# Performance work log

Hardware: AMD Instinct MI355X
Metric: run time of the kernel (lower is better)

## Reference

```python
import jax, jax.numpy as jnp
import numpy as np

H, W = 1280, 1920          # dense depth canvas (hardcoded in the torch module)
OUT_H, OUT_W = 427, 640    # kornia resize target
BIG = 1e9                  # sentinel coordinate for 'no seed yet'
FX = FY = 1000.0
CX, CY = 960.0, 640.0


def _jfa_nearest(valid):
    """1+JFA jump-flooding: (H,W) bool -> (H,W,2) float coords of nearest valid pixel.
    Replaces the faiss GpuIndexFlatL2 exact 1-NN over pixel coordinates."""
    rr, cc = jnp.meshgrid(jnp.arange(H, dtype=jnp.float32),
                          jnp.arange(W, dtype=jnp.float32), indexing='ij')
    coords = jnp.stack([rr, cc], axis=-1)                      # (H,W,2)
    nearest = jnp.where(valid[..., None], coords, BIG)
    best = jnp.sum((coords - nearest) ** 2, axis=-1)           # squared dist to current seed
    row_idx = jnp.arange(H)[:, None]
    col_idx = jnp.arange(W)[None, :]
    steps = [1, 1024, 512, 256, 128, 64, 32, 16, 8, 4, 2, 1]   # 1+JFA schedule, max dim 1920
    for k in steps:
        for dy in (-k, 0, k):
            for dx in (-k, 0, k):
                if dy == 0 and dx == 0:
                    continue
                cand = jnp.roll(nearest, (dy, dx), axis=(0, 1))
                src_r = row_idx - dy
                src_c = col_idx - dx
                ok = (src_r >= 0) & (src_r < H) & (src_c >= 0) & (src_c < W)
                cand = jnp.where(ok[..., None], cand, BIG)
                d = jnp.sum((coords - cand) ** 2, axis=-1)
                better = d < best
                best = jnp.where(better, d, best)
                nearest = jnp.where(better[..., None], cand, nearest)
    return nearest


def _one(points, pose, extrinsic, intrinsic):
    # projection path uses points.detach() in the torch code -> stop_gradient here
    p = jax.lax.stop_gradient(points)
    pts_world = p @ pose[:3, :3].T + pose[:3, 3]
    cam = pts_world @ extrinsic[:3, :3].T + extrinsic[:3, 3]
    proj = cam @ intrinsic.T
    u = proj[:, 0] / proj[:, 2]
    v = proj[:, 1] / proj[:, 2]
    r = jnp.floor(v).astype(jnp.int32)   # indices[..., [1,0]] swap -> row = v
    c = jnp.floor(u).astype(jnp.int32)
    depth_vals = jnp.linalg.norm(points, axis=-1)   # differentiable wrt points
    mask = (r >= 0) & (r < H) & (c >= 0) & (c < W)
    rs = jnp.where(mask, r, 0)
    cs = jnp.where(mask, c, 0)
    vals = jnp.where(mask, depth_vals, 0.0)
    # sparse scatter -> dense (duplicates sum, like torch.sparse to_dense)
    depth = jnp.zeros((H, W), jnp.float32).at[rs, cs].add(vals)
    valid = depth != 0
    nearest = jax.lax.stop_gradient(_jfa_nearest(valid))   # integer NN indices: non-diff
    nr = jnp.clip(nearest[..., 0], 0, H - 1).astype(jnp.int32)
    nc = jnp.clip(nearest[..., 1], 0, W - 1).astype(jnp.int32)
    rrf = jnp.arange(H, dtype=jnp.float32)[:, None]
    ccf = jnp.arange(W, dtype=jnp.float32)[None, :]
    dist = jnp.sqrt((rrf - nr.astype(jnp.float32)) ** 2 + (ccf - nc.astype(jnp.float32)) ** 2)
    dist = jnp.where(valid, 0.0, dist)          # dist_matrix only written at invalid pixels
    filled = jnp.where(valid, depth, depth[nr, nc])  # depth*(1-mask) + interpolated*mask
    out = jnp.stack([filled, dist], axis=0)     # (2, H, W)
    return jax.image.resize(out, (2, OUT_H, OUT_W), method='linear')


_batched = jax.jit(jax.vmap(_one))


def setup_inputs() -> dict:
    key = jax.random.key(0)
    B, N = 2, 120000
    ku, kv, kd = jax.random.split(key, 3)
    # sample pixels + depths, back-project so points land on the canvas
    u = jax.random.uniform(ku, (B, N), minval=0.0, maxval=W - 1.0)
    v = jax.random.uniform(kv, (B, N), minval=0.0, maxval=H - 1.0)
    d = jax.random.uniform(kd, (B, N), minval=2.0, maxval=50.0)
    x = (u - CX) * d / FX
    y = (v - CY) * d / FY
    points = jnp.stack([x, y, d], axis=-1).astype(jnp.float32)
    eye4 = jnp.broadcast_to(jnp.eye(4, dtype=jnp.float32), (B, 4, 4))
    K = jnp.array([[FX, 0.0, CX], [0.0, FY, CY], [0.0, 0.0, 1.0]], jnp.float32)
    intrinsic = jnp.broadcast_to(K, (B, 3, 3))
    return {"points": points, "pose": eye4, "extrinsic": eye4, "intrinsic": intrinsic}


def reference(points, pose, extrinsic, intrinsic):
    return _batched(points, pose, extrinsic, intrinsic)   # (B, 2, 427, 640)
```

## Files before the change

### kernel.cpp

```cpp
#include <hip/hip_runtime.h>
#include <math.h>
#include <limits.h>

#define HH 1280
#define WW 1920
#define OUT_H 427
#define OUT_W 640
#define SENT 0x7fff7fff

typedef short short2v __attribute__((ext_vector_type(2)));

__device__ __forceinline__ int dot22(int a, int P) {
#if __has_builtin(__builtin_amdgcn_sdot2)
    short2v s = __builtin_bit_cast(short2v, a) - __builtin_bit_cast(short2v, P);
    return __builtin_amdgcn_sdot2(s, s, 0, false);
#else
    int dr = (a >> 16) - (P >> 16);
    int dc = (short)a - (short)P;
    return dr * dr + dc * dc;
#endif
}
#define PICK(P, cur, dcur, cand)                    \
    {                                               \
        int _d = dot22((cand), (P));                \
        if (_d < (dcur)) { (cur) = (cand); (dcur) = _d; } \
    }

__global__ void scatter_k(const float* __restrict__ pts,
                          const float* __restrict__ pose,
                          const float* __restrict__ extr,
                          const float* __restrict__ intr,
                          float* __restrict__ depth, int N) {
    #pragma clang fp contract(off)
    int t = blockIdx.x * blockDim.x + threadIdx.x;
    int b = blockIdx.y;
    if (t >= N) return;
    const float* p = pts + ((long)b * N + t) * 3;
    float x = p[0], y = p[1], z = p[2];
    const float* P = pose + b * 16;
    const float* E = extr + b * 16;
    const float* K = intr + b * 9;
    float wx = ((x*P[0] + y*P[1]) + z*P[2]) + P[3];
    float wy = ((x*P[4] + y*P[5]) + z*P[6]) + P[7];
    float wz = ((x*P[8] + y*P[9]) + z*P[10]) + P[11];
    float cx = ((wx*E[0] + wy*E[1]) + wz*E[2]) + E[3];
    float cy = ((wx*E[4] + wy*E[5]) + wz*E[6]) + E[7];
    float cz = ((wx*E[8] + wy*E[9]) + wz*E[10]) + E[11];
    float px = (cx*K[0] + cy*K[1]) + cz*K[2];
    float py = (cx*K[3] + cy*K[4]) + cz*K[5];
    float pz = (cx*K[6] + cy*K[7]) + cz*K[8];
    float u = px / pz, v = py / pz;
    int r = (int)floorf(v), c = (int)floorf(u);
    if (r >= 0 && r < HH && c >= 0 && c < WW) {
        float dv = sqrtf((x*x + y*y) + z*z);
        atomicAdd(depth + ((long)b * HH + r) * WW + c, dv);
    }
}

template <bool FIRST>
__global__ __launch_bounds__(512)
void jfa3r_k(const void* __restrict__ inv_, int* __restrict__ out, int dy, int k) {
    __shared__ int rows[4][WW];
    int i = blockIdx.x, b = blockIdx.y;
    if (FIRST) {
        const float* dep = (const float*)inv_ + (long)b * HH * WW;
        #pragma unroll
        for (int t = 0; t < 4; ++t) {
            int r = i - t * dy;
            if (r >= 0 && r < HH) {
                const float4* src = reinterpret_cast<const float4*>(dep + (long)r * WW);
                for (int c4 = threadIdx.x; c4 < WW / 4; c4 += 512) {
                    float4 d = src[c4];
                    int4 v;
                    int c0 = c4 * 4, pb = r << 16;
                    v.x = (d.x != 0.0f) ? (pb | c0)       : SENT;
                    v.y = (d.y != 0.0f) ? (pb | (c0 + 1)) : SENT;
                    v.z = (d.z != 0.0f) ? (pb | (c0 + 2)) : SENT;
                    v.w = (d.w != 0.0f) ? (pb | (c0 + 3)) : SENT;
                    reinterpret_cast<int4*>(rows[t])[c4] = v;
                }
            } else {
                int4 sv; sv.x = sv.y = sv.z = sv.w = SENT;
                for (int c4 = threadIdx.x; c4 < WW / 4; c4 += 512)
                    reinterpret_cast<int4*>(rows[t])[c4] = sv;
            }
        }
    } else {
        const int* im = (const int*)inv_ + (long)b * HH * WW;
        #pragma unroll
        for (int t = 0; t < 4; ++t) {
            int r = i - t * dy;
            if (r >= 0 && r < HH) {
                const int4* src = reinterpret_cast<const int4*>(im + (long)r * WW);
                for (int c4 = threadIdx.x; c4 < WW / 4; c4 += 512)
                    reinterpret_cast<int4*>(rows[t])[c4] = src[c4];
            } else {
                int4 sv; sv.x = sv.y = sv.z = sv.w = SENT;
                for (int c4 = threadIdx.x; c4 < WW / 4; c4 += 512)
                    reinterpret_cast<int4*>(rows[t])[c4] = sv;
            }
        }
    }
    __syncthreads();
    bool rv1 = (unsigned)(i - dy)     < (unsigned)HH;
    bool rv2 = (unsigned)(i - 2 * dy) < (unsigned)HH;
    int* orow = out + ((long)b * HH + i) * WW;
    for (int j = threadIdx.x; j < WW; j += 512) {
        bool jk = (j + k < WW);
        int Pp = (i << 16) | j;
        int cur = rows[0][j];
        int dcur = dot22(cur, Pp);
        int c1 = jk ? rows[1][j + k] : SENT;
        PICK(Pp, cur, dcur, c1)
        int o1m = SENT;
        if (rv1) {
            int Pm = ((i - dy) << 16) | j;
            int a = rows[1][j];
            int da = dot22(a, Pm);
            int c2 = jk ? rows[2][j + k] : SENT;
            PICK(Pm, a, da, c2)
            o1m = a;
        }
        PICK(Pp, cur, dcur, o1m)
        int o2q = SENT;
        int qj = j - k;
        if (rv1 && qj >= 0) {
            int Pq = ((i - dy) << 16) | qj;
            int a0 = rows[1][qj];
            int d0 = dot22(a0, Pq);
            PICK(Pq, a0, d0, rows[2][j])
            int a1 = SENT;
            if (rv2) {
                int Pq2 = ((i - 2 * dy) << 16) | qj;
                a1 = rows[2][qj];
                int d1 = dot22(a1, Pq2);
                PICK(Pq2, a1, d1, rows[3][j])
            }
            PICK(Pq, a0, d0, a1)
            o2q = a0;
        }
        PICK(Pp, cur, dcur, o2q)
        orow[j] = cur;
    }
}

__global__ __launch_bounds__(512)
void jfa2r_k(const int* __restrict__ in, int* __restrict__ out, int k) {
    __shared__ int row[WW];
    int i = blockIdx.x, b = blockIdx.y;
    const int4* src = reinterpret_cast<const int4*>(in + ((long)b * HH + i) * WW);
    for (int c4 = threadIdx.x; c4 < WW / 4; c4 += 512)
        reinterpret_cast<int4*>(row)[c4] = src[c4];
    __syncthreads();
    int* orow = out + ((long)b * HH + i) * WW;
    for (int j = threadIdx.x; j < WW; j += 512) {
        int Pp = (i << 16) | j;
        int a = row[j];
        int cur = a;
        int dcur = dot22(cur, Pp);
        int apk = (j + k < WW) ? row[j + k] : SENT;
        PICK(Pp, cur, dcur, apk)
        int o1m = SENT;
        int qj = j - k;
        if (qj >= 0) {
            int Pm = (i << 16) | qj;
            int am = row[qj];
            int dm = dot22(am, Pm);
            PICK(Pm, am, dm, a)
            o1m = am;
        }
        PICK(Pp, cur, dcur, o1m)
        orow[j] = cur;
    }
}

__global__ __launch_bounds__(256)
void hresize_k(const float* __restrict__ depth,
               const int* __restrict__ nr,
               float* __restrict__ tmp) {
    __shared__ float fbuf[WW];
    __shared__ float dbuf[WW];
    int i = blockIdx.x, b = blockIdx.y;
    const float* dep = depth + (long)b * HH * WW;
    const float* drow = dep + (long)i * WW;
    const int* nrow = nr + ((long)b * HH + i) * WW;
    for (int j = threadIdx.x; j < WW; j += 256) {
        float dv = drow[j];
        float f, dist;
        if (dv != 0.0f) { f = dv; dist = 0.0f; }
        else {
            int nn = nrow[j];
            int rr, cc;
            if (nn == SENT) { rr = HH - 1; cc = WW - 1; }
            else { rr = nn >> 16; cc = nn & 0xffff; }
            f = dep[(long)rr * WW + cc];
            float drr = (float)i - (float)rr, dcc = (float)j - (float)cc;
            dist = sqrtf(drr * drr + dcc * dcc);
        }
        fbuf[j] = f; dbuf[j] = dist;
    }
    __syncthreads();
    const float inv = 3.0f;
    for (int ow = threadIdx.x; ow < OUT_W; ow += 256) {
        float sf = (ow + 0.5f) * inv - 0.5f;
        int i0 = (int)ceilf(sf - inv);
        float a0 = 0.f, a1 = 0.f, wsum = 0.f;
        for (int k = 0; k < 7; ++k) {
            int iw = i0 + k;
            if (iw < 0 || iw >= WW) continue;
            float wgt = 1.0f - fabsf(sf - (float)iw) / inv;
            if (wgt <= 0.0f) continue;
            a0 += wgt * fbuf[iw]; a1 += wgt * dbuf[iw]; wsum += wgt;
        }
        long o = (((long)b * 2 + 0) * HH + i) * OUT_W + ow;
        tmp[o] = a0 / wsum;
        tmp[o + (long)HH * OUT_W] = a1 / wsum;
    }
}

__global__ void vresize_k(const float* __restrict__ tmp, float* __restrict__ out) {
    int ow = blockIdx.x * blockDim.x + threadIdx.x;
    int oh = blockIdx.y, bc = blockIdx.z;
    if (ow >= OUT_W) return;
    const float inv = (float)(1280.0 / 427.0);
    float sf = (oh + 0.5f) * inv - 0.5f;
    int i0 = (int)ceilf(sf - inv);
    float acc = 0.f, wsum = 0.f;
    const float* src = tmp + (long)bc * HH * OUT_W;
    for (int k = 0; k < 7; ++k) {
        int ih = i0 + k;
        if (ih < 0 || ih >= HH) continue;
        float wgt = 1.0f - fabsf(sf - (float)ih) / inv;
        if (wgt <= 0.0f) continue;
        acc += wgt * src[(long)ih * OUT_W + ow];
        wsum += wgt;
    }
    out[((long)bc * OUT_H + oh) * OUT_W + ow] = acc / wsum;
}

extern "C" void kernel_launch(void* const* d_in, const int* in_sizes, int n_in,
                              void* d_out, int out_size, void* d_ws, size_t ws_size,
                              hipStream_t stream) {
    const float* pts  = (const float*)d_in[0];
    const float* pose = (const float*)d_in[1];
    const float* extr = (const float*)d_in[2];
    const float* intr = (const float*)d_in[3];
    int B = in_sizes[1] / 16;
    int N = in_sizes[0] / (3 * B);

    char* ws = (char*)d_ws;
    size_t imgSz = (size_t)B * HH * WW;
    float* depth = (float*)ws;
    int*   nearA = (int*)(ws + imgSz * 4);
    int*   nearB = (int*)(ws + imgSz * 8);
    float* tmp   = (float*)(ws + imgSz * 12);

    hipMemsetAsync(depth, 0, imgSz * sizeof(float), stream);

    dim3 bs(256);
    scatter_k<<<dim3((N + 255) / 256, B), bs, 0, stream>>>(pts, pose, extr, intr, depth, N);

    dim3 gr(HH, B);
    int* cur = nearA; int* nxt = nearB;
    jfa3r_k<true><<<gr, 512, 0, stream>>>(depth, cur, -1, 1);
    jfa2r_k<<<gr, 512, 0, stream>>>(cur, nxt, 1);
    { int* t2 = cur; cur = nxt; nxt = t2; }
    jfa3r_k<false><<<gr, 512, 0, stream>>>(cur, nxt, +1, 1);
    { int* t2 = cur; cur = nxt; nxt = t2; }

    const int steps_rest[11] = {1024, 512, 256, 128, 64, 32, 16, 8, 4, 2, 1};
    for (int s = 0; s < 11; ++s) {
        int k = steps_rest[s];
        jfa3r_k<false><<<gr, 512, 0, stream>>>(cur, nxt, -k, k);
        { int* t2 = cur; cur = nxt; nxt = t2; }
        jfa2r_k<<<gr, 512, 0, stream>>>(cur, nxt, k);
        { int* t2 = cur; cur = nxt; nxt = t2; }
        jfa3r_k<false><<<gr, 512, 0, stream>>>(cur, nxt, +k, k);
        { int* t2 = cur; cur = nxt; nxt = t2; }
    }

    hresize_k<<<dim3(HH, B), bs, 0, stream>>>(depth, cur, tmp);
    vresize_k<<<dim3((OUT_W + 255) / 256, OUT_H, B * 2), bs, 0, stream>>>(tmp, (float*)d_out);
}
```

Measured before the change: 563.1 us.

## Fuse downward-row JFA pass with same-row pass in one kernel

The first vertical JFA sub-pass (looking at rows i+k, i+2k, i+3k) and the horizontal same-row sub-pass are merged into one kernel. The intermediate row stays in shared memory instead of being written to and re-read from global memory. This removes one launch and one full-image read and write per JFA step, 12 steps in total. The cost is extra shared memory per block (an added row buffer), which may lower occupancy.

```diff
diff --git a/kernel.cpp b/kernel.cpp
--- a/kernel.cpp
+++ b/kernel.cpp
@@ -57,17 +57,19 @@
     }
 }
 
+
 template <bool FIRST>
 __global__ __launch_bounds__(512)
-void jfa3r_k(const void* __restrict__ inv_, int* __restrict__ out, int dy, int k) {
+void jfa12_k(const void* __restrict__ inv_, int* __restrict__ out, int k) {
     __shared__ int rows[4][WW];
+    __shared__ int g1row[WW];
     int i = blockIdx.x, b = blockIdx.y;
     if (FIRST) {
         const float* dep = (const float*)inv_ + (long)b * HH * WW;
         #pragma unroll
         for (int t = 0; t < 4; ++t) {
-            int r = i - t * dy;
-            if (r >= 0 && r < HH) {
+            int r = i + t * k;
+            if (r < HH) {
                 const float4* src = reinterpret_cast<const float4*>(dep + (long)r * WW);
                 for (int c4 = threadIdx.x; c4 < WW / 4; c4 += 512) {
                     float4 d = src[c4];
@@ -89,8 +91,8 @@
         const int* im = (const int*)inv_ + (long)b * HH * WW;
         #pragma unroll
         for (int t = 0; t < 4; ++t) {
-            int r = i - t * dy;
-            if (r >= 0 && r < HH) {
+            int r = i + t * k;
+            if (r < HH) {
                 const int4* src = reinterpret_cast<const int4*>(im + (long)r * WW);
                 for (int c4 = threadIdx.x; c4 < WW / 4; c4 += 512)
                     reinterpret_cast<int4*>(rows[t])[c4] = src[c4];
@@ -99,6 +101,87 @@
                 for (int c4 = threadIdx.x; c4 < WW / 4; c4 += 512)
                     reinterpret_cast<int4*>(rows[t])[c4] = sv;
             }
+        }
+    }
+    __syncthreads();
+    bool rv1 = (i + k)     < HH;
+    bool rv2 = (i + 2 * k) < HH;
+    for (int j = threadIdx.x; j < WW; j += 512) {
+        bool jk = (j + k < WW);
+        int Pp = (i << 16) | j;
+        int cur = rows[0][j];
+        int dcur = dot22(cur, Pp);
+        int c1 = jk ? rows[1][j + k] : SENT;
+        PICK(Pp, cur, dcur, c1)
+        int o1m = SENT;
+        if (rv1) {
+            int Pm = ((i + k) << 16) | j;
+            int a = rows[1][j];
+            int da = dot22(a, Pm);
+            int c2 = jk ? rows[2][j + k] : SENT;
+            PICK(Pm, a, da, c2)
+            o1m = a;
+        }
+        PICK(Pp, cur, dcur, o1m)
+        int o2q = SENT;
+        int qj = j - k;
+        if (rv1 && qj >= 0) {
+            int Pq = ((i + k) << 16) | qj;
+            int a0 = rows[1][qj];
+            int d0 = dot22(a0, Pq);
+            PICK(Pq, a0, d0, rows[2][j])
+            int a1 = SENT;
+            if (rv2) {
+                int Pq2 = ((i + 2 * k) << 16) | qj;
+                a1 = rows[2][qj];
+                int d1 = dot22(a1, Pq2);
+                PICK(Pq2, a1, d1, rows[3][j])
+            }
+            PICK(Pq, a0, d0, a1)
+            o2q = a0;
+        }
+        PICK(Pp, cur, dcur, o2q)
+        g1row[j] = cur;
+    }
+    __syncthreads();
+    int* orow = out + ((long)b * HH + i) * WW;
+    for (int j = threadIdx.x; j < WW; j += 512) {
+        int Pp = (i << 16) | j;
+        int a = g1row[j];
+        int cur = a;
+        int dcur = dot22(cur, Pp);
+        int apk = (j + k < WW) ? g1row[j + k] : SENT;
+        PICK(Pp, cur, dcur, apk)
+        int o1m = SENT;
+        int qj = j - k;
+        if (qj >= 0) {
+            int Pm = (i << 16) | qj;
+            int am = g1row[qj];
+            int dm = dot22(am, Pm);
+            PICK(Pm, am, dm, a)
+            o1m = am;
+        }
+        PICK(Pp, cur, dcur, o1m)
+        orow[j] = cur;
+    }
+}
+
+__global__ __launch_bounds__(512)
+void jfa3r_k(const int* __restrict__ inv_, int* __restrict__ out, int dy, int k) {
+    __shared__ int rows[4][WW];
+    int i = blockIdx.x, b = blockIdx.y;
+    const int* im = inv_ + (long)b * HH * WW;
+    #pragma unroll
+    for (int t = 0; t < 4; ++t) {
+        int r = i - t * dy;
+        if (r >= 0 && r < HH) {
+            const int4* src = reinterpret_cast<const int4*>(im + (long)r * WW);
+            for (int c4 = threadIdx.x; c4 < WW / 4; c4 += 512)
+                reinterpret_cast<int4*>(rows[t])[c4] = src[c4];
+        } else {
+            int4 sv; sv.x = sv.y = sv.z = sv.w = SENT;
+            for (int c4 = threadIdx.x; c4 < WW / 4; c4 += 512)
+                reinterpret_cast<int4*>(rows[t])[c4] = sv;
         }
     }
     __syncthreads();
@@ -140,36 +223,6 @@
             o2q = a0;
         }
         PICK(Pp, cur, dcur, o2q)
-        orow[j] = cur;
-    }
-}
-
-__global__ __launch_bounds__(512)
-void jfa2r_k(const int* __restrict__ in, int* __restrict__ out, int k) {
-    __shared__ int row[WW];
-    int i = blockIdx.x, b = blockIdx.y;
-    const int4* src = reinterpret_cast<const int4*>(in + ((long)b * HH + i) * WW);
-    for (int c4 = threadIdx.x; c4 < WW / 4; c4 += 512)
-        reinterpret_cast<int4*>(row)[c4] = src[c4];
-    __syncthreads();
-    int* orow = out + ((long)b * HH + i) * WW;
-    for (int j = threadIdx.x; j < WW; j += 512) {
-        int Pp = (i << 16) | j;
-        int a = row[j];
-        int cur = a;
-        int dcur = dot22(cur, Pp);
-        int apk = (j + k < WW) ? row[j + k] : SENT;
-        PICK(Pp, cur, dcur, apk)
-        int o1m = SENT;
-        int qj = j - k;
-        if (qj >= 0) {
-            int Pm = (i << 16) | qj;
-            int am = row[qj];
-            int dm = dot22(am, Pm);
-            PICK(Pm, am, dm, a)
-            o1m = am;
-        }
-        PICK(Pp, cur, dcur, o1m)
         orow[j] = cur;
     }
 }
@@ -262,20 +315,16 @@
 
     dim3 gr(HH, B);
     int* cur = nearA; int* nxt = nearB;
-    jfa3r_k<true><<<gr, 512, 0, stream>>>(depth, cur, -1, 1);
-    jfa2r_k<<<gr, 512, 0, stream>>>(cur, nxt, 1);
-    { int* t2 = cur; cur = nxt; nxt = t2; }
-    jfa3r_k<false><<<gr, 512, 0, stream>>>(cur, nxt, +1, 1);
+    jfa12_k<true><<<gr, 512, 0, stream>>>(depth, cur, 1);
+    jfa3r_k<<<gr, 512, 0, stream>>>(cur, nxt, +1, 1);
     { int* t2 = cur; cur = nxt; nxt = t2; }
 
     const int steps_rest[11] = {1024, 512, 256, 128, 64, 32, 16, 8, 4, 2, 1};
     for (int s = 0; s < 11; ++s) {
         int k = steps_rest[s];
-        jfa3r_k<false><<<gr, 512, 0, stream>>>(cur, nxt, -k, k);
+        jfa12_k<false><<<gr, 512, 0, stream>>>(cur, nxt, k);
         { int* t2 = cur; cur = nxt; nxt = t2; }
-        jfa2r_k<<<gr, 512, 0, stream>>>(cur, nxt, k);
-        { int* t2 = cur; cur = nxt; nxt = t2; }
-        jfa3r_k<false><<<gr, 512, 0, stream>>>(cur, nxt, +k, k);
+        jfa3r_k<<<gr, 512, 0, stream>>>(cur, nxt, +k, k);
         { int* t2 = cur; cur = nxt; nxt = t2; }
     }
 
```

New measurement: 497.4 us. -11.7%, faster.
